# Performance work log

Measured on AMD Instinct MI355X. Metric: run time of the kernel, lower is better.

Reference implementation:

```python
import jax, jax.numpy as jnp
import numpy as np

B, S, DIM = 2, 2048, 4096
NH, NKV, HD = 32, 8, 128
N_REP = NH // NKV


def setup_inputs() -> dict:
    key = jax.random.key(0)
    ks = jax.random.split(key, 6)
    scale = 0.02
    x = jax.random.normal(ks[0], (B, S, DIM), dtype=jnp.float32)
    # RoPE table: angles[s, i] = s / 10000^(2i/HD); stored as (cos, sin) pairs
    inv_freq = 1.0 / (10000.0 ** (np.arange(0, HD, 2, dtype=np.float32) / HD))
    ang = np.arange(S, dtype=np.float32)[:, None] * inv_freq[None, :]  # [S, HD/2]
    freqs_cis = jnp.asarray(np.stack([np.cos(ang), np.sin(ang)], axis=-1), dtype=jnp.float32)
    wq = jax.random.normal(ks[1], (DIM, NH * HD), dtype=jnp.float32) * scale
    wk = jax.random.normal(ks[2], (DIM, NKV * HD), dtype=jnp.float32) * scale
    wv = jax.random.normal(ks[3], (DIM, NKV * HD), dtype=jnp.float32) * scale
    wo = jax.random.normal(ks[4], (NH * HD, DIM), dtype=jnp.float32) * scale
    return {"x": x, "freqs_cis": freqs_cis, "wq": wq, "wk": wk, "wv": wv, "wo": wo}


def _apply_rope(xh, fc):
    # xh: [B, S, H, HD]; fc: [S, HD/2, 2] (cos, sin). Pairs are consecutive dims
    # (matches torch view_as_complex on reshape(..., -1, 2)). Done in fp32.
    b, s, h, d = xh.shape
    xp = xh.astype(jnp.float32).reshape(b, s, h, d // 2, 2)
    cos = fc[:, None, :, 0]  # [S, 1, HD/2] -> broadcasts over batch & heads
    sin = fc[:, None, :, 1]
    xr, xi = xp[..., 0], xp[..., 1]
    out_r = xr * cos - xi * sin
    out_i = xr * sin + xi * cos
    return jnp.stack([out_r, out_i], axis=-1).reshape(b, s, h, d).astype(xh.dtype)


def reference(x, freqs_cis, wq, wk, wv, wo):
    b, s, _ = x.shape
    xq = (x @ wq).reshape(b, s, NH, HD)
    xk = (x @ wk).reshape(b, s, NKV, HD)
    xv = (x @ wv).reshape(b, s, NKV, HD)
    xq = _apply_rope(xq, freqs_cis)
    xk = _apply_rope(xk, freqs_cis)
    new_k, new_v = xk, xv  # kv_cache is None -> new cache is this step's K/V

    # GQA: group query heads [NH] as [NKV, N_REP]; no K/V materialized repeat.
    q = xq.transpose(0, 2, 1, 3).reshape(b, NKV, N_REP, s, HD)
    k = xk.transpose(0, 2, 1, 3)  # [B, NKV, S, HD]
    v = xv.transpose(0, 2, 1, 3)
    scores = jnp.einsum("bgrqd,bgkd->bgrqk", q, k) / jnp.sqrt(jnp.float32(HD))
    attn = jax.nn.softmax(scores, axis=-1)  # is_causal=False -> full attention
    ctx = jnp.einsum("bgrqk,bgkd->bgrqd", attn, v)  # [B, NKV, N_REP, S, HD]
    ctx = ctx.reshape(b, NH, s, HD).transpose(0, 2, 1, 3).reshape(b, s, NH * HD)
    out = ctx @ wo
    return out, new_k, new_v
```

## Files before the change

kernel.cpp:

```cpp
#include <hip/hip_runtime.h>
#include <hip/hip_bf16.h>
#include <math.h>

#define B_    2
#define S_    2048
#define DIM_  4096
#define NH_   32
#define NKV_  8
#define HD_   128
#define NREP_ 4

typedef __attribute__((ext_vector_type(8))) short bf16x8;
typedef __attribute__((ext_vector_type(4))) float floatx4;

__device__ __forceinline__ unsigned short f2bf(float f) {
    unsigned int u = __float_as_uint(f);
    unsigned int r = (u + 0x7FFFu + ((u >> 16) & 1u)) >> 16;
    return (unsigned short)r;
}
__device__ __forceinline__ float bf2f(unsigned short u) {
    return __uint_as_float((unsigned int)u << 16);
}
__device__ __forceinline__ unsigned int cvt_pk_bf16(float lo, float hi) {
    unsigned int r;
    asm("v_cvt_pk_bf16_f32 %0, %1, %2" : "=v"(r) : "v"(lo), "v"(hi));
    return r;
}
__device__ __forceinline__ float rowmax16(float x) {
    int t;
    t = __builtin_amdgcn_mov_dpp(__float_as_int(x), 0x121, 0xf, 0xf, true);
    x = fmaxf(x, __int_as_float(t));
    t = __builtin_amdgcn_mov_dpp(__float_as_int(x), 0x122, 0xf, 0xf, true);
    x = fmaxf(x, __int_as_float(t));
    t = __builtin_amdgcn_mov_dpp(__float_as_int(x), 0x124, 0xf, 0xf, true);
    x = fmaxf(x, __int_as_float(t));
    t = __builtin_amdgcn_mov_dpp(__float_as_int(x), 0x128, 0xf, 0xf, true);
    x = fmaxf(x, __int_as_float(t));
    return x;
}
__device__ __forceinline__ void gload_lds16(const unsigned short* g, unsigned short* l) {
    __builtin_amdgcn_global_load_lds(
        (const __attribute__((address_space(1))) void*)g,
        (__attribute__((address_space(3))) void*)l, 16, 0, 0);
}

__global__ __launch_bounds__(256)
void convert_bf16(const float* __restrict__ in, unsigned short* __restrict__ out,
                  long long n) {
    long long i = ((long long)blockIdx.x * 256 + threadIdx.x) * 4;
    if (i >= n) return;
    const float4 v = *(const float4*)(in + i);
    ushort4 o;
    o.x = f2bf(v.x); o.y = f2bf(v.y); o.z = f2bf(v.z); o.w = f2bf(v.w);
    *(ushort4*)(out + i) = o;
}

__global__ __launch_bounds__(256)
void transpose_conv(const float* __restrict__ W, unsigned short* __restrict__ Wt,
                    int K, int N) {
    __shared__ unsigned short t[32][33];
    const int tx = threadIdx.x & 31, ty = threadIdx.x >> 5;
    const int n0 = blockIdx.x * 32, k0 = blockIdx.y * 32;
    for (int i = 0; i < 4; ++i)
        t[ty + i * 8][tx] = f2bf(W[(size_t)(k0 + ty + i * 8) * N + n0 + tx]);
    __syncthreads();
    for (int i = 0; i < 4; ++i)
        Wt[(size_t)(n0 + ty + i * 8) * K + k0 + tx] = t[tx][ty + i * 8];
}

template<bool OUT_BF16>
__global__ __launch_bounds__(256)
void gemm_bt(const unsigned short* __restrict__ A,
             const unsigned short* __restrict__ Bt,
             void* __restrict__ C, int M, int N, int K) {
    __shared__ unsigned short As[128 * 32];
    __shared__ unsigned short Bs[128 * 32];
    const int tid  = threadIdx.x;
    const int lane = tid & 63;
    const int wave = tid >> 6;
    const int l16  = lane & 15;
    const int quad = lane >> 4;
    const int tileM = blockIdx.x * 128, tileN = blockIdx.y * 128;
    const int waveM = (wave >> 1) * 64, waveN = (wave & 1) * 64;

    floatx4 acc[4][4] = {};

    const int r0 = tid >> 2, ko = (tid & 3) * 8;

    for (int k0 = 0; k0 < K; k0 += 32) {
        for (int p = 0; p < 2; ++p) {
            const int idx = p * 256 + tid;
            const int row = r0 + p * 64;
            gload_lds16(A  + (size_t)(tileM + row) * K + k0 + ko, &As[idx * 8]);
            gload_lds16(Bt + (size_t)(tileN + row) * K + k0 + ko, &Bs[idx * 8]);
        }
        __syncthreads();
        bf16x8 af[4], bfr[4];
        for (int i = 0; i < 4; ++i) {
            af[i]  = *(const bf16x8*)&As[(waveM + i * 16 + l16) * 32 + quad * 8];
            bfr[i] = *(const bf16x8*)&Bs[(waveN + i * 16 + l16) * 32 + quad * 8];
        }
        for (int mi = 0; mi < 4; ++mi)
            for (int ni = 0; ni < 4; ++ni)
                acc[mi][ni] = __builtin_amdgcn_mfma_f32_16x16x32_bf16(
                    af[mi], bfr[ni], acc[mi][ni], 0, 0, 0);
        __syncthreads();
    }
    for (int mi = 0; mi < 4; ++mi)
        for (int r = 0; r < 4; ++r) {
            const int row = tileM + waveM + mi * 16 + quad * 4 + r;
            for (int ni = 0; ni < 4; ++ni) {
                const int col = tileN + waveN + ni * 16 + l16;
                if (OUT_BF16)
                    ((unsigned short*)C)[(size_t)row * N + col] = f2bf(acc[mi][ni][r]);
                else
                    ((float*)C)[(size_t)row * N + col] = acc[mi][ni][r];
            }
        }
}

__global__ __launch_bounds__(256)
void gemm_kv(const unsigned short* __restrict__ A,
             const unsigned short* __restrict__ Bt,
             float* __restrict__ Ck,
             float* __restrict__ Cv,
             int M, int K) {
    __shared__ unsigned short As[128 * 32];
    __shared__ unsigned short Bs[128 * 32];
    const int tid  = threadIdx.x;
    const int lane = tid & 63;
    const int wave = tid >> 6;
    const int l16  = lane & 15;
    const int quad = lane >> 4;
    const int tileM = blockIdx.x * 128, tileN = blockIdx.y * 128;
    const int waveM = (wave >> 1) * 64, waveN = (wave & 1) * 64;

    floatx4 acc[4][4] = {};
    const int r0 = tid >> 2, ko = (tid & 3) * 8;

    for (int k0 = 0; k0 < K; k0 += 32) {
        for (int p = 0; p < 2; ++p) {
            const int idx = p * 256 + tid;
            const int row = r0 + p * 64;
            gload_lds16(A  + (size_t)(tileM + row) * K + k0 + ko, &As[idx * 8]);
            gload_lds16(Bt + (size_t)(tileN + row) * K + k0 + ko, &Bs[idx * 8]);
        }
        __syncthreads();
        bf16x8 af[4], bfr[4];
        for (int i = 0; i < 4; ++i) {
            af[i]  = *(const bf16x8*)&As[(waveM + i * 16 + l16) * 32 + quad * 8];
            bfr[i] = *(const bf16x8*)&Bs[(waveN + i * 16 + l16) * 32 + quad * 8];
        }
        for (int mi = 0; mi < 4; ++mi)
            for (int ni = 0; ni < 4; ++ni)
                acc[mi][ni] = __builtin_amdgcn_mfma_f32_16x16x32_bf16(
                    af[mi], bfr[ni], acc[mi][ni], 0, 0, 0);
        __syncthreads();
    }
    float* const Cd = (tileN < NKV_ * HD_) ? Ck : Cv;
    const int colBase = tileN < NKV_ * HD_ ? tileN : tileN - NKV_ * HD_;
    for (int mi = 0; mi < 4; ++mi)
        for (int r = 0; r < 4; ++r) {
            const int row = tileM + waveM + mi * 16 + quad * 4 + r;
            for (int ni = 0; ni < 4; ++ni) {
                const int col = colBase + waveN + ni * 16 + l16;
                Cd[(size_t)row * (NKV_ * HD_) + col] = acc[mi][ni][r];
            }
        }
}

__global__ __launch_bounds__(256)
void rope2(unsigned short* __restrict__ qio, const float* __restrict__ xk,
           const float* __restrict__ nv, const float* __restrict__ fc,
           unsigned short* __restrict__ kb, unsigned short* __restrict__ vtb,
           float* __restrict__ new_k) {
    const long long QP = (long long)B_ * S_ * NH_ * (HD_ / 2);
    const long long KP = (long long)B_ * S_ * NKV_ * (HD_ / 2);
    const long long idx = (long long)blockIdx.x * 256 + threadIdx.x;
    if (idx < QP) {
        const int d2 = (int)(idx & 63);
        const long long rh = idx >> 6;
        const int s = (int)((rh / NH_) % S_);
        const ushort2 u = *(const ushort2*)(qio + idx * 2);
        const float xr = bf2f(u.x), xi = bf2f(u.y);
        const float cs = fc[((size_t)s * 64 + d2) * 2];
        const float sn = fc[((size_t)s * 64 + d2) * 2 + 1];
        *(ushort2*)(qio + idx * 2) =
            make_ushort2(f2bf(xr * cs - xi * sn), f2bf(xr * sn + xi * cs));
    } else if (idx < QP + KP) {
        const long long e = idx - QP;
        const int d2 = (int)(e & 63);
        const long long rh = e >> 6;
        const int g = (int)(rh & (NKV_ - 1));
        const long long row = rh >> 3;
        const int b = (int)(row / S_), s = (int)(row % S_);
        const float2 v = *(const float2*)(xk + e * 2);
        const float cs = fc[((size_t)s * 64 + d2) * 2];
        const float sn = fc[((size_t)s * 64 + d2) * 2 + 1];
        const float orr = v.x * cs - v.y * sn;
        const float oii = v.x * sn + v.y * cs;
        *(float2*)(new_k + e * 2) = make_float2(orr, oii);
        const size_t kbi = ((size_t)(b * NKV_ + g) * S_ + s) * HD_ + d2 * 2;
        *(ushort2*)(kb + kbi) = make_ushort2(f2bf(orr), f2bf(oii));
    } else if (idx < QP + 2 * KP) {
        const long long e = idx - QP - KP;
        const float2 v = *(const float2*)(nv + e * 2);
        const long long fe = e * 2;
        const int c = (int)(fe & (HD_ - 1));
        const long long rh = fe >> 7;
        const int g = (int)(rh & (NKV_ - 1));
        const long long row = rh >> 3;
        const int b = (int)(row / S_), s = (int)(row % S_);
        const size_t base = ((size_t)(b * NKV_ + g) * HD_ + c) * S_ + s;
        vtb[base]      = f2bf(v.x);
        vtb[base + S_] = f2bf(v.y);
    }
}

__global__ __launch_bounds__(256)
void flash_attn(const unsigned short* __restrict__ qb,
                const unsigned short* __restrict__ kb,
                const unsigned short* __restrict__ vtb,
                unsigned short* __restrict__ ctxb) {
    __shared__ unsigned short Ks[2][64 * 128];
    __shared__ unsigned short Vs[2][128 * 64];
    __shared__ unsigned short Plds[4][16 * 72];
    const int tid  = threadIdx.x;
    const int wave = tid >> 6, lane = tid & 63;
    const int l16  = lane & 15, quad = lane >> 4;
    const int bi  = blockIdx.x;
    const int qt4 = bi & (S_ / 64 - 1);
    const int bh  = bi >> 5;
    const int h = bh & (NH_ - 1), b = bh >> 5;
    const int g = h >> 2;
    const int qt = qt4 * 4 + wave;
    const float sc2 = 0.12754857629633723f;

    const unsigned short* kbase = kb  + (size_t)(b * NKV_ + g) * S_ * HD_;
    const unsigned short* vbase = vtb + (size_t)(b * NKV_ + g) * HD_ * S_;

    bf16x8 qf[4];
    {
        const unsigned short* qp =
            qb + ((size_t)(b * S_ + qt * 16 + l16) * NH_ + h) * HD_;
        for (int c = 0; c < 4; ++c) qf[c] = *(const bf16x8*)(qp + c * 32 + quad * 8);
    }

    float m_i[4], l_p[4];
    for (int r = 0; r < 4; ++r) { m_i[r] = -1e30f; l_p[r] = 0.f; }
    floatx4 oacc[8] = {};
    unsigned short* pw = &Plds[wave][0];

    auto stage = [&](int buf, int kt) {
        for (int rnd = 0; rnd < 4; ++rnd) {
            const int ci = rnd * 256 + tid;
            const int row = ci >> 4, c = ci & 15;
            gload_lds16(kbase + (size_t)(kt + row) * HD_ + (c ^ (row & 15)) * 8,
                        &Ks[buf][ci * 8]);
        }
        for (int rnd = 0; rnd < 4; ++rnd) {
            const int ci = rnd * 256 + tid;
            const int row = ci >> 3, c = ci & 7;
            gload_lds16(vbase + (size_t)row * S_ + kt + (c ^ (row & 7)) * 8,
                        &Vs[buf][ci * 8]);
        }
    };

    stage(0, 0);
    __syncthreads();

    int cur = 0;
    for (int kt = 0; kt < S_; kt += 64) {
        if (kt + 64 < S_) stage(cur ^ 1, kt + 64);
        floatx4 sacc[4] = {};
        __builtin_amdgcn_s_setprio(1);
        for (int t = 0; t < 4; ++t) {
            const int row = t * 16 + l16;
            const char* kp = (const char*)&Ks[cur][row * 128];
            for (int c = 0; c < 4; ++c) {
                const bf16x8 kf = *(const bf16x8*)
                    (kp + ((c * 64 + quad * 16) ^ (l16 << 4)));
                sacc[t] = __builtin_amdgcn_mfma_f32_16x16x32_bf16(qf[c], kf, sacc[t], 0, 0, 0);
            }
        }
        __builtin_amdgcn_s_setprio(0);
        float sv[4][4], mx[4];
        for (int r = 0; r < 4; ++r) {
            const float s0 = sacc[0][r] * sc2, s1 = sacc[1][r] * sc2;
            const float s2 = sacc[2][r] * sc2, s3 = sacc[3][r] * sc2;
            sv[0][r] = s0; sv[1][r] = s1; sv[2][r] = s2; sv[3][r] = s3;
            mx[r] = rowmax16(fmaxf(fmaxf(s0, s1), fmaxf(s2, s3)));
        }
        const bool ok = (mx[0] <= m_i[0] + 8.f) && (mx[1] <= m_i[1] + 8.f) &&
                        (mx[2] <= m_i[2] + 8.f) && (mx[3] <= m_i[3] + 8.f);
        if (__all(ok)) {
            for (int r = 0; r < 4; ++r) {
                const float e0 = __builtin_amdgcn_exp2f(sv[0][r] - m_i[r]);
                const float e1 = __builtin_amdgcn_exp2f(sv[1][r] - m_i[r]);
                const float e2 = __builtin_amdgcn_exp2f(sv[2][r] - m_i[r]);
                const float e3 = __builtin_amdgcn_exp2f(sv[3][r] - m_i[r]);
                l_p[r] += (e0 + e1) + (e2 + e3);
                const int ro = (quad * 4 + r) * 72 + l16;
                const unsigned int p01 = cvt_pk_bf16(e0, e1);
                const unsigned int p23 = cvt_pk_bf16(e2, e3);
                pw[ro]      = (unsigned short)p01;
                pw[ro + 16] = (unsigned short)(p01 >> 16);
                pw[ro + 32] = (unsigned short)p23;
                pw[ro + 48] = (unsigned short)(p23 >> 16);
            }
        } else {
            float alpha[4];
            for (int r = 0; r < 4; ++r) {
                const float mnew = fmaxf(m_i[r], mx[r]);
                const float a  = __builtin_amdgcn_exp2f(m_i[r] - mnew);
                const float e0 = __builtin_amdgcn_exp2f(sv[0][r] - mnew);
                const float e1 = __builtin_amdgcn_exp2f(sv[1][r] - mnew);
                const float e2 = __builtin_amdgcn_exp2f(sv[2][r] - mnew);
                const float e3 = __builtin_amdgcn_exp2f(sv[3][r] - mnew);
                l_p[r] = l_p[r] * a + (e0 + e1) + (e2 + e3);
                m_i[r] = mnew;
                alpha[r] = a;
                const int ro = (quad * 4 + r) * 72 + l16;
                const unsigned int p01 = cvt_pk_bf16(e0, e1);
                const unsigned int p23 = cvt_pk_bf16(e2, e3);
                pw[ro]      = (unsigned short)p01;
                pw[ro + 16] = (unsigned short)(p01 >> 16);
                pw[ro + 32] = (unsigned short)p23;
                pw[ro + 48] = (unsigned short)(p23 >> 16);
            }
            for (int f = 0; f < 8; ++f)
                for (int r = 0; r < 4; ++r) oacc[f][r] *= alpha[r];
        }
        asm volatile("s_waitcnt lgkmcnt(0)" ::: "memory");
        __builtin_amdgcn_s_setprio(1);
        for (int t2 = 0; t2 < 2; ++t2) {
            const bf16x8 pf = *(const bf16x8*)&pw[l16 * 72 + t2 * 32 + quad * 8];
            for (int f = 0; f < 8; ++f) {
                const int row = f * 16 + l16;
                const bf16x8 vf = *(const bf16x8*)((const char*)&Vs[cur][row * 64]
                                   + ((t2 * 64 + quad * 16) ^ ((l16 & 7) << 4)));
                oacc[f] = __builtin_amdgcn_mfma_f32_16x16x32_bf16(pf, vf, oacc[f], 0, 0, 0);
            }
        }
        __builtin_amdgcn_s_setprio(0);
        __syncthreads();
        cur ^= 1;
    }
    for (int r = 0; r < 4; ++r) {
        float l = l_p[r];
        for (int off = 1; off < 16; off <<= 1) l += __shfl_xor(l, off);
        const float inv = 1.0f / l;
        const int srow = qt * 16 + quad * 4 + r;
        unsigned short* cp = ctxb + ((size_t)(b * S_ + srow) * NH_ + h) * HD_ + l16;
        for (int f = 0; f < 8; ++f) cp[f * 16] = f2bf(oacc[f][r] * inv);
    }
}

extern "C" void kernel_launch(void* const* d_in, const int* in_sizes, int n_in,
                              void* d_out, int out_size, void* d_ws, size_t ws_size,
                              hipStream_t stream) {
    const float* x  = (const float*)d_in[0];
    const float* fc = (const float*)d_in[1];
    const float* wq = (const float*)d_in[2];
    const float* wk = (const float*)d_in[3];
    const float* wv = (const float*)d_in[4];
    const float* wo = (const float*)d_in[5];

    float* out   = (float*)d_out;
    float* new_k = out + (size_t)B_ * S_ * NH_ * HD_;
    float* new_v = new_k + (size_t)B_ * S_ * NKV_ * HD_;

    char* ws = (char*)d_ws;
    unsigned short* xb   = (unsigned short*)(ws);
    unsigned short* wqT  = (unsigned short*)(ws + (32ull  << 20));
    unsigned short* wkT  = (unsigned short*)(ws + (64ull  << 20));
    unsigned short* wvT  = (unsigned short*)(ws + (72ull  << 20));
    unsigned short* xqb  = (unsigned short*)(ws + (80ull  << 20));
    float*          xk   = (float*)         (ws + (112ull << 20));
    unsigned short* kbuf = (unsigned short*)(ws + (128ull << 20));
    unsigned short* vtb  = (unsigned short*)(ws + (136ull << 20));
    unsigned short* ctxb = xb;
    unsigned short* woT  = wqT;

    const int M = B_ * S_;
    dim3 blk(256);

    convert_bf16<<<(int)(((size_t)M * DIM_ / 4 + 255) / 256), blk, 0, stream>>>(
        x, xb, (long long)M * DIM_);
    transpose_conv<<<dim3(DIM_ / 32, DIM_ / 32), blk, 0, stream>>>(wq, wqT, DIM_, DIM_);
    transpose_conv<<<dim3((NKV_ * HD_) / 32, DIM_ / 32), blk, 0, stream>>>(wk, wkT, DIM_, NKV_ * HD_);
    transpose_conv<<<dim3((NKV_ * HD_) / 32, DIM_ / 32), blk, 0, stream>>>(wv, wvT, DIM_, NKV_ * HD_);

    gemm_bt<true ><<<dim3(M / 128, (NH_  * HD_) / 128), blk, 0, stream>>>(xb, wqT, xqb, M, NH_ * HD_, DIM_);
    gemm_kv<<<dim3(M / 128, (2 * NKV_ * HD_) / 128), blk, 0, stream>>>(xb, wkT, xk, new_v, M, DIM_);

    transpose_conv<<<dim3(DIM_ / 32, DIM_ / 32), blk, 0, stream>>>(wo, woT, DIM_, DIM_);

    const long long totalPairs = (long long)B_ * S_ * (HD_ / 2) * (NH_ + 2 * NKV_);
    rope2<<<(int)((totalPairs + 255) / 256), blk, 0, stream>>>(
        xqb, xk, new_v, fc, kbuf, vtb, new_k);

    flash_attn<<<B_ * NH_ * (S_ / 64), blk, 0, stream>>>(xqb, kbuf, vtb, ctxb);

    gemm_bt<false><<<dim3(M / 128, DIM_ / 128), blk, 0, stream>>>(ctxb, woT, out, M, DIM_, DIM_);
}
```

Before: 1.069 ms.

## Process two query tiles per wave in flash attention to reuse K/V tiles

Each wave now handles two 16-row query tiles instead of one, so each block covers 128 query rows and the grid is halved. Every K and V tile staged into shared memory feeds twice as many MFMAs, which halves global K/V traffic and LDS staging per unit of work. The cost is higher register use (two sets of output accumulators and softmax state), which can lower occupancy, and fewer blocks (1024) to fill the GPU.

Result: slower. 1.164 ms (+8.8%).

```diff
diff --git a/kernel.cpp b/kernel.cpp
--- a/kernel.cpp
+++ b/kernel.cpp
@@ -229,26 +229,33 @@
     const int wave = tid >> 6, lane = tid & 63;
     const int l16  = lane & 15, quad = lane >> 4;
     const int bi  = blockIdx.x;
-    const int qt4 = bi & (S_ / 64 - 1);
-    const int bh  = bi >> 5;
+    const int qt8 = bi & (S_ / 128 - 1);
+    const int bh  = bi >> 4;
     const int h = bh & (NH_ - 1), b = bh >> 5;
     const int g = h >> 2;
-    const int qt = qt4 * 4 + wave;
+    const int qtA = qt8 * 8 + wave;
+    const int qtB = qtA + 4;
     const float sc2 = 0.12754857629633723f;
 
     const unsigned short* kbase = kb  + (size_t)(b * NKV_ + g) * S_ * HD_;
     const unsigned short* vbase = vtb + (size_t)(b * NKV_ + g) * HD_ * S_;
 
-    bf16x8 qf[4];
+    bf16x8 qfA[4], qfB[4];
     {
-        const unsigned short* qp =
-            qb + ((size_t)(b * S_ + qt * 16 + l16) * NH_ + h) * HD_;
-        for (int c = 0; c < 4; ++c) qf[c] = *(const bf16x8*)(qp + c * 32 + quad * 8);
-    }
-
-    float m_i[4], l_p[4];
-    for (int r = 0; r < 4; ++r) { m_i[r] = -1e30f; l_p[r] = 0.f; }
-    floatx4 oacc[8] = {};
+        const unsigned short* qpA =
+            qb + ((size_t)(b * S_ + qtA * 16 + l16) * NH_ + h) * HD_;
+        const unsigned short* qpB =
+            qb + ((size_t)(b * S_ + qtB * 16 + l16) * NH_ + h) * HD_;
+        for (int c = 0; c < 4; ++c) {
+            qfA[c] = *(const bf16x8*)(qpA + c * 32 + quad * 8);
+            qfB[c] = *(const bf16x8*)(qpB + c * 32 + quad * 8);
+        }
+    }
+
+    float mA[4], lA[4], mB[4], lB[4];
+    for (int r = 0; r < 4; ++r) { mA[r] = -1e30f; lA[r] = 0.f;
+                                  mB[r] = -1e30f; lB[r] = 0.f; }
+    floatx4 oA[8] = {}, oB[8] = {};
     unsigned short* pw = &Plds[wave][0];
 
     auto stage = [&](int buf, int kt) {
@@ -272,7 +279,7 @@
     int cur = 0;
     for (int kt = 0; kt < S_; kt += 64) {
         if (kt + 64 < S_) stage(cur ^ 1, kt + 64);
-        floatx4 sacc[4] = {};
+        floatx4 sA[4] = {}, sB[4] = {};
         __builtin_amdgcn_s_setprio(1);
         for (int t = 0; t < 4; ++t) {
             const int row = t * 16 + l16;
@@ -280,79 +287,95 @@
             for (int c = 0; c < 4; ++c) {
                 const bf16x8 kf = *(const bf16x8*)
                     (kp + ((c * 64 + quad * 16) ^ (l16 << 4)));
-                sacc[t] = __builtin_amdgcn_mfma_f32_16x16x32_bf16(qf[c], kf, sacc[t], 0, 0, 0);
+                sA[t] = __builtin_amdgcn_mfma_f32_16x16x32_bf16(qfA[c], kf, sA[t], 0, 0, 0);
+                sB[t] = __builtin_amdgcn_mfma_f32_16x16x32_bf16(qfB[c], kf, sB[t], 0, 0, 0);
             }
         }
         __builtin_amdgcn_s_setprio(0);
-        float sv[4][4], mx[4];
-        for (int r = 0; r < 4; ++r) {
-            const float s0 = sacc[0][r] * sc2, s1 = sacc[1][r] * sc2;
-            const float s2 = sacc[2][r] * sc2, s3 = sacc[3][r] * sc2;
-            sv[0][r] = s0; sv[1][r] = s1; sv[2][r] = s2; sv[3][r] = s3;
-            mx[r] = rowmax16(fmaxf(fmaxf(s0, s1), fmaxf(s2, s3)));
-        }
-        const bool ok = (mx[0] <= m_i[0] + 8.f) && (mx[1] <= m_i[1] + 8.f) &&
-                        (mx[2] <= m_i[2] + 8.f) && (mx[3] <= m_i[3] + 8.f);
-        if (__all(ok)) {
+
+        auto smpv = [&](floatx4 (&sacc)[4], float (&m_i)[4], float (&l_p)[4],
+                        floatx4 (&oacc)[8]) {
+            float sv[4][4], mx[4];
             for (int r = 0; r < 4; ++r) {
-                const float e0 = __builtin_amdgcn_exp2f(sv[0][r] - m_i[r]);
-                const float e1 = __builtin_amdgcn_exp2f(sv[1][r] - m_i[r]);
-                const float e2 = __builtin_amdgcn_exp2f(sv[2][r] - m_i[r]);
-                const float e3 = __builtin_amdgcn_exp2f(sv[3][r] - m_i[r]);
-                l_p[r] += (e0 + e1) + (e2 + e3);
-                const int ro = (quad * 4 + r) * 72 + l16;
-                const unsigned int p01 = cvt_pk_bf16(e0, e1);
-                const unsigned int p23 = cvt_pk_bf16(e2, e3);
-                pw[ro]      = (unsigned short)p01;
-                pw[ro + 16] = (unsigned short)(p01 >> 16);
-                pw[ro + 32] = (unsigned short)p23;
-                pw[ro + 48] = (unsigned short)(p23 >> 16);
-            }
-        } else {
-            float alpha[4];
-            for (int r = 0; r < 4; ++r) {
-                const float mnew = fmaxf(m_i[r], mx[r]);
-                const float a  = __builtin_amdgcn_exp2f(m_i[r] - mnew);
-                const float e0 = __builtin_amdgcn_exp2f(sv[0][r] - mnew);
-                const float e1 = __builtin_amdgcn_exp2f(sv[1][r] - mnew);
-                const float e2 = __builtin_amdgcn_exp2f(sv[2][r] - mnew);
-                const float e3 = __builtin_amdgcn_exp2f(sv[3][r] - mnew);
-                l_p[r] = l_p[r] * a + (e0 + e1) + (e2 + e3);
-                m_i[r] = mnew;
-                alpha[r] = a;
-                const int ro = (quad * 4 + r) * 72 + l16;
-                const unsigned int p01 = cvt_pk_bf16(e0, e1);
-                const unsigned int p23 = cvt_pk_bf16(e2, e3);
-                pw[ro]      = (unsigned short)p01;
-                pw[ro + 16] = (unsigned short)(p01 >> 16);
-                pw[ro + 32] = (unsigned short)p23;
-                pw[ro + 48] = (unsigned short)(p23 >> 16);
-            }
-            for (int f = 0; f < 8; ++f)
-                for (int r = 0; r < 4; ++r) oacc[f][r] *= alpha[r];
-        }
-        asm volatile("s_waitcnt lgkmcnt(0)" ::: "memory");
-        __builtin_amdgcn_s_setprio(1);
-        for (int t2 = 0; t2 < 2; ++t2) {
-            const bf16x8 pf = *(const bf16x8*)&pw[l16 * 72 + t2 * 32 + quad * 8];
-            for (int f = 0; f < 8; ++f) {
-                const int row = f * 16 + l16;
-                const bf16x8 vf = *(const bf16x8*)((const char*)&Vs[cur][row * 64]
-                                   + ((t2 * 64 + quad * 16) ^ ((l16 & 7) << 4)));
-                oacc[f] = __builtin_amdgcn_mfma_f32_16x16x32_bf16(pf, vf, oacc[f], 0, 0, 0);
-            }
-        }
-        __builtin_amdgcn_s_setprio(0);
+                const float s0 = sacc[0][r] * sc2, s1 = sacc[1][r] * sc2;
+                const float s2 = sacc[2][r] * sc2, s3 = sacc[3][r] * sc2;
+                sv[0][r] = s0; sv[1][r] = s1; sv[2][r] = s2; sv[3][r] = s3;
+                mx[r] = rowmax16(fmaxf(fmaxf(s0, s1), fmaxf(s2, s3)));
+            }
+            const bool ok = (mx[0] <= m_i[0] + 8.f) && (mx[1] <= m_i[1] + 8.f) &&
+                            (mx[2] <= m_i[2] + 8.f) && (mx[3] <= m_i[3] + 8.f);
+            if (__all(ok)) {
+                for (int r = 0; r < 4; ++r) {
+                    const float e0 = __builtin_amdgcn_exp2f(sv[0][r] - m_i[r]);
+                    const float e1 = __builtin_amdgcn_exp2f(sv[1][r] - m_i[r]);
+                    const float e2 = __builtin_amdgcn_exp2f(sv[2][r] - m_i[r]);
+                    const float e3 = __builtin_amdgcn_exp2f(sv[3][r] - m_i[r]);
+                    l_p[r] += (e0 + e1) + (e2 + e3);
+                    const int ro = (quad * 4 + r) * 72 + l16;
+                    const unsigned int p01 = cvt_pk_bf16(e0, e1);
+                    const unsigned int p23 = cvt_pk_bf16(e2, e3);
+                    pw[ro]      = (unsigned short)p01;
+                    pw[ro + 16] = (unsigned short)(p01 >> 16);
+                    pw[ro + 32] = (unsigned short)p23;
+                    pw[ro + 48] = (unsigned short)(p23 >> 16);
+                }
+            } else {
+                float alpha[4];
+                for (int r = 0; r < 4; ++r) {
+                    const float mnew = fmaxf(m_i[r], mx[r]);
+                    const float a  = __builtin_amdgcn_exp2f(m_i[r] - mnew);
+                    const float e0 = __builtin_amdgcn_exp2f(sv[0][r] - mnew);
+                    const float e1 = __builtin_amdgcn_exp2f(sv[1][r] - mnew);
+                    const float e2 = __builtin_amdgcn_exp2f(sv[2][r] - mnew);
+                    const float e3 = __builtin_amdgcn_exp2f(sv[3][r] - mnew);
+                    l_p[r] = l_p[r] * a + (e0 + e1) + (e2 + e3);
+                    m_i[r] = mnew;
+                    alpha[r] = a;
+                    const int ro = (quad * 4 + r) * 72 + l16;
+                    const unsigned int p01 = cvt_pk_bf16(e0, e1);
+                    const unsigned int p23 = cvt_pk_bf16(e2, e3);
+                    pw[ro]      = (unsigned short)p01;
+                    pw[ro + 16] = (unsigned short)(p01 >> 16);
+                    pw[ro + 32] = (unsigned short)p23;
+                    pw[ro + 48] = (unsigned short)(p23 >> 16);
+                }
+                for (int f = 0; f < 8; ++f)
+                    for (int r = 0; r < 4; ++r) oacc[f][r] *= alpha[r];
+            }
+            asm volatile("s_waitcnt lgkmcnt(0)" ::: "memory");
+            __builtin_amdgcn_s_setprio(1);
+            for (int t2 = 0; t2 < 2; ++t2) {
+                const bf16x8 pf = *(const bf16x8*)&pw[l16 * 72 + t2 * 32 + quad * 8];
+                for (int f = 0; f < 8; ++f) {
+                    const int row = f * 16 + l16;
+                    const bf16x8 vf = *(const bf16x8*)((const char*)&Vs[cur][row * 64]
+                                       + ((t2 * 64 + quad * 16) ^ ((l16 & 7) << 4)));
+                    oacc[f] = __builtin_amdgcn_mfma_f32_16x16x32_bf16(pf, vf, oacc[f], 0, 0, 0);
+                }
+            }
+            __builtin_amdgcn_s_setprio(0);
+        };
+        smpv(sA, mA, lA, oA);
+        smpv(sB, mB, lB, oB);
+
         __syncthreads();
         cur ^= 1;
     }
     for (int r = 0; r < 4; ++r) {
-        float l = l_p[r];
+        float l = lA[r];
         for (int off = 1; off < 16; off <<= 1) l += __shfl_xor(l, off);
         const float inv = 1.0f / l;
-        const int srow = qt * 16 + quad * 4 + r;
+        const int srow = qtA * 16 + quad * 4 + r;
         unsigned short* cp = ctxb + ((size_t)(b * S_ + srow) * NH_ + h) * HD_ + l16;
-        for (int f = 0; f < 8; ++f) cp[f * 16] = f2bf(oacc[f][r] * inv);
+        for (int f = 0; f < 8; ++f) cp[f * 16] = f2bf(oA[f][r] * inv);
+    }
+    for (int r = 0; r < 4; ++r) {
+        float l = lB[r];
+        for (int off = 1; off < 16; off <<= 1) l += __shfl_xor(l, off);
+        const float inv = 1.0f / l;
+        const int srow = qtB * 16 + quad * 4 + r;
+        unsigned short* cp = ctxb + ((size_t)(b * S_ + srow) * NH_ + h) * HD_ + l16;
+        for (int f = 0; f < 8; ++f) cp[f * 16] = f2bf(oB[f][r] * inv);
     }
 }
 
@@ -400,7 +423,7 @@
     rope2<<<(int)((totalPairs + 255) / 256), blk, 0, stream>>>(
         xqb, xk, new_v, fc, kbuf, vtb, new_k);
 
-    flash_attn<<<B_ * NH_ * (S_ / 64), blk, 0, stream>>>(xqb, kbuf, vtb, ctxb);
+    flash_attn<<<B_ * NH_ * (S_ / 128), blk, 0, stream>>>(xqb, kbuf, vtb, ctxb);
 
     gemm_bt<false><<<dim3(M / 128, DIM_ / 128), blk, 0, stream>>>(ctxb, woT, out, M, DIM_, DIM_);
 }
```
